# Performance work log

Measured on AMD Instinct MI355X. Metric: run time of the kernel, lower is better.

## Reference

```python
import jax, jax.numpy as jnp
import numpy as np

CH = 64
SCALE = 2
GROUPS = 4
K = 3
GN_GROUPS = min(CH // 8, 8)  # = 8
EPS_GN = 1e-5
EPS_COS = 1e-8


def setup_inputs() -> dict:
    key = jax.random.key(0)
    ks = jax.random.split(key, 4)
    B, H, W = 8, 256, 256
    OC = 2 * GROUPS
    lap = jnp.array([[0., -1., 0.], [-1., 4., -1.], [0., -1., 0.]], dtype=jnp.float32)
    hp_weight = jnp.tile(lap[None, None], (CH, 1, 1, 1))  # depthwise high-pass kernel
    return {
        "x": jax.random.normal(ks[0], (B, CH, H, W), dtype=jnp.float32),
        "gn_gamma": jnp.ones((CH,), jnp.float32),
        "gn_beta": jnp.zeros((CH,), jnp.float32),
        "hp_weight": hp_weight,
        "dir_w": jax.random.normal(ks[1], (OC, K * K - 1), jnp.float32) * 0.001,
        "dir_b": jnp.zeros((OC,), jnp.float32),
        "mag_w": jax.random.normal(ks[2], (OC, CH), jnp.float32) * 0.02,
        "mag_b": jnp.zeros((OC,), jnp.float32),
        "hfg_w": jax.random.normal(ks[3], (OC, CH), jnp.float32) * 0.02,
        "hfg_b": jnp.zeros((OC,), jnp.float32),
    }


def group_norm(x, gamma, beta, g, eps=EPS_GN):
    B, C, H, W = x.shape
    xr = x.reshape(B, g, -1)
    mu = xr.mean(-1, keepdims=True)
    var = xr.var(-1, keepdims=True)
    xn = ((xr - mu) * jax.lax.rsqrt(var + eps)).reshape(B, C, H, W)
    return xn * gamma[None, :, None, None] + beta[None, :, None, None]


def dw_conv3(x, w):
    # depthwise 3x3, padding=1, no bias
    return jax.lax.conv_general_dilated(
        x, w, window_strides=(1, 1), padding=((1, 1), (1, 1)),
        dimension_numbers=("NCHW", "OIHW", "NCHW"), feature_group_count=x.shape[1])


def avg_pool(x, s):
    B, C, H, W = x.shape
    return x.reshape(B, C, H // s, s, W // s, s).mean(axis=(3, 5))


def direction_feat(x, k=K):
    # cosine similarity (over channels) of center pixel vs each of k*k neighbors, center dropped
    B, C, H, W = x.shape
    p = k // 2
    xp = jnp.pad(x, ((0, 0), (0, 0), (p, p), (p, p)))
    patches = jnp.stack([xp[:, :, i:i + H, j:j + W]
                         for i in range(k) for j in range(k)], axis=2)  # [B,C,k2,H,W]
    center = patches[:, :, k * k // 2:k * k // 2 + 1]  # [B,C,1,H,W]
    dot = (center * patches).sum(axis=1)               # [B,k2,H,W]
    n1 = jnp.sqrt((center * center).sum(axis=1))       # [B,1,H,W]
    n2 = jnp.sqrt((patches * patches).sum(axis=1))     # [B,k2,H,W]
    sim = dot / (jnp.maximum(n1, EPS_COS) * jnp.maximum(n2, EPS_COS))
    c = k * k // 2
    return jnp.concatenate([sim[:, :c], sim[:, c + 1:]], axis=1)  # [B,k2-1,H,W]


def conv1x1(w, b, x):
    return jnp.einsum("oc,bchw->bohw", w, x) + b[None, :, None, None]


def grid_sample_border(x, grid):
    # x: [N,C,H,W]; grid: [N,Hg,Wg,2] in [-1,1]; bilinear, align_corners=False, padding_mode='border'
    N, C, H, W = x.shape
    gx, gy = grid[..., 0], grid[..., 1]
    ix = jnp.clip(((gx + 1.0) * W - 1.0) * 0.5, 0.0, W - 1.0)
    iy = jnp.clip(((gy + 1.0) * H - 1.0) * 0.5, 0.0, H - 1.0)
    x0 = jnp.floor(ix); y0 = jnp.floor(iy)
    wx = (ix - x0)[..., None]; wy = (iy - y0)[..., None]
    x0i = jnp.clip(x0.astype(jnp.int32), 0, W - 1)
    y0i = jnp.clip(y0.astype(jnp.int32), 0, H - 1)
    x1i = jnp.clip(x0i + 1, 0, W - 1)
    y1i = jnp.clip(y0i + 1, 0, H - 1)
    img = x.transpose(0, 2, 3, 1)  # [N,H,W,C]
    b = jnp.arange(N)[:, None, None]
    v00 = img[b, y0i, x0i]; v01 = img[b, y0i, x1i]
    v10 = img[b, y1i, x0i]; v11 = img[b, y1i, x1i]
    out = (v00 * (1 - wx) * (1 - wy) + v01 * wx * (1 - wy)
           + v10 * (1 - wx) * wy + v11 * wx * wy)
    return out.transpose(0, 3, 1, 2)  # [N,C,Hg,Wg]


def reference(x, gn_gamma, gn_beta, hp_weight, dir_w, dir_b, mag_w, mag_b, hfg_w, hfg_b):
    B, C, H, W = x.shape
    xn = group_norm(x, gn_gamma, gn_beta, GN_GROUPS)
    hf = dw_conv3(xn, hp_weight)
    xl = avg_pool(xn, SCALE)
    hfl = avg_pool(hf, SCALE)
    df = direction_feat(xl)
    gate = jax.nn.sigmoid(conv1x1(mag_w, mag_b, xl) + conv1x1(hfg_w, hfg_b, hfl))
    offset = conv1x1(dir_w, dir_b, df) * gate  # [B, 2*GROUPS, Hl, Wl]
    Hl, Wl = H // SCALE, W // SCALE
    off = offset.reshape(B, 2, GROUPS, Hl, Wl)
    cy = jnp.arange(Hl, dtype=x.dtype) * SCALE + SCALE / 2.0  # high-res pixel centers
    cx = jnp.arange(Wl, dtype=x.dtype) * SCALE + SCALE / 2.0
    gx = (cx[None, None, None, :] + off[:, 0]) * (2.0 / W) - 1.0  # [B,G,Hl,Wl]
    gy = (cy[None, None, :, None] + off[:, 1]) * (2.0 / H) - 1.0
    grid = jnp.stack([gx, gy], axis=-1).reshape(B * GROUPS, Hl, Wl, 2)
    xg = x.reshape(B * GROUPS, C // GROUPS, H, W)
    out = grid_sample_border(xg, grid)
    return out.reshape(B, C, Hl, Wl)
```

## Files before the change

kernel.cpp:

```cpp
#include <hip/hip_runtime.h>
#include <hip/hip_bf16.h>
#include <math.h>

#define B_ 8
#define C_ 64
#define H_ 256
#define W_ 256
#define HL_ 128
#define WL_ 128
#define GN_G 8
#define CPG 8
#define GRP 4
#define OC_ 8
#define GROUP_ELEMS (CPG * H_ * W_)

#define TILE_H 16
#define XROWS 34
#define LDSW 264

__global__ __launch_bounds__(256) void k2_fused(const float* __restrict__ x,
                                                const float* __restrict__ hpw,
                                                float* __restrict__ px,
                                                float* __restrict__ pL,
                                                float* __restrict__ partials) {
  __shared__ float tile[XROWS * LDSW];
  __shared__ float rs[4], rs2[4];
  const int t = threadIdx.x;
  const int blk = blockIdx.x;
  const int tileIdx = blk & 7;
  const int bc = blk >> 3;
  const int c = bc & 63;
  const int hl0 = tileIdx * TILE_H;
  const float* plane = x + (size_t)bc * (H_ * W_);
  const int y0 = 2 * hl0 - 1;

  if (t < XROWS * 2) {
    const int r = t >> 1;
    tile[r * LDSW + ((t & 1) ? 260 : 3)] = 0.f;
  }

  float s = 0.f, s2 = 0.f;
  for (int i = 0; i < 9; ++i) {
    const int q = t + i * 256;
    if (q >= XROWS * 64) break;
    const int r = q >> 6;
    const int c4 = (q & 63) << 2;
    const int y = y0 + r;
    float4 v = make_float4(0.f, 0.f, 0.f, 0.f);
    if ((unsigned)y < (unsigned)H_)
      v = *reinterpret_cast<const float4*>(plane + y * W_ + c4);
    *reinterpret_cast<float4*>(&tile[r * LDSW + 4 + c4]) = v;
    if (r >= 1 && r <= 32) {
      s  += v.x + v.y + v.z + v.w;
      s2 += v.x * v.x + v.y * v.y + v.z * v.z + v.w * v.w;
    }
  }
#pragma unroll
  for (int off = 32; off > 0; off >>= 1) {
    s  += __shfl_down(s, off, 64);
    s2 += __shfl_down(s2, off, 64);
  }
  if ((t & 63) == 0) { rs[t >> 6] = s; rs2[t >> 6] = s2; }
  __syncthreads();
  if (t == 0) {
    partials[blk * 2 + 0] = rs[0] + rs[1] + rs[2] + rs[3];
    partials[blk * 2 + 1] = rs2[0] + rs2[1] + rs2[2] + rs2[3];
  }

  float w[9];
#pragma unroll
  for (int i = 0; i < 9; ++i) w[i] = hpw[c * 9 + i];

  const int wl = t & 127;
  const int hs = (t >> 7) * 8;
  const int colb = 3 + 2 * wl;
  const int rbase = 2 * hs;
  float win[4][4];
#pragma unroll
  for (int j = 0; j < 4; ++j)
#pragma unroll
    for (int d = 0; d < 4; ++d)
      win[j][d] = tile[(rbase + j) * LDSW + colb + d];

  int outIdx = (bc * HL_ + (hl0 + hs)) * WL_ + wl;
#pragma unroll
  for (int i = 0; i < 8; ++i) {
    float pr[4][3];
#pragma unroll
    for (int j = 0; j < 4; ++j)
#pragma unroll
      for (int d = 0; d < 3; ++d) pr[j][d] = win[j][d] + win[j][d + 1];
    float hfsum = 0.f;
    float q11 = 0.f;
#pragma unroll
    for (int j = 0; j < 3; ++j)
#pragma unroll
      for (int d = 0; d < 3; ++d) {
        const float qq = pr[j][d] + pr[j + 1][d];
        hfsum = fmaf(w[j * 3 + d], qq, hfsum);
        if (j == 1 && d == 1) q11 = qq;
      }
    px[outIdx] = 0.25f * q11;
    pL[outIdx] = 0.25f * hfsum;
    outIdx += WL_;
    if (i < 7) {
      const int rn = rbase + 2 * i + 4;
#pragma unroll
      for (int d = 0; d < 4; ++d) {
        win[0][d] = win[2][d];
        win[1][d] = win[3][d];
        win[2][d] = tile[rn * LDSW + colb + d];
        win[3][d] = tile[(rn + 1) * LDSW + colb + d];
      }
    }
  }
}

__global__ __launch_bounds__(512) void k1_finish(const float* __restrict__ partials,
                                                 const float* __restrict__ gamma,
                                                 const float* __restrict__ beta,
                                                 float* __restrict__ ab) {
  const int t = threadIdx.x;
  const int b = t >> 6, c = t & 63, g = c >> 3;
  float S = 0.f, S2 = 0.f;
  for (int c2 = g * CPG; c2 < g * CPG + CPG; ++c2)
#pragma unroll
    for (int p = 0; p < 8; ++p) {
      const int blk = (b * 64 + c2) * 8 + p;
      S  += partials[blk * 2 + 0];
      S2 += partials[blk * 2 + 1];
    }
  const float N = (float)GROUP_ELEMS;
  const float mean = S / N;
  const float var = fmaxf(S2 / N - mean * mean, 0.f);
  const float a = rsqrtf(var + 1e-5f) * gamma[c];
  ab[t * 2 + 0] = a;
  ab[t * 2 + 1] = beta[c] - mean * a;
}

#define TS 16
__global__ __launch_bounds__(256) void k3_offset(const float* __restrict__ px,
                                                 const float* __restrict__ pL,
                                                 const float* __restrict__ ab,
                                                 const float* __restrict__ dir_w,
                                                 const float* __restrict__ dir_b,
                                                 const float* __restrict__ mag_w,
                                                 const float* __restrict__ mag_b,
                                                 const float* __restrict__ hfg_w,
                                                 const float* __restrict__ hfg_b,
                                                 float2* __restrict__ grid) {
  __shared__ float s_v[2][16][18][24];
  __shared__ float s_mw[C_][OC_];
  __shared__ float s_hw[C_][OC_];
  __shared__ float s_dir[OC_][8];
  __shared__ float s_ab2[C_][2];
  __shared__ float s_bias[2][OC_];

  const int tid = threadIdx.x;
  const int bx = blockIdx.x;
  const int tx = bx & 7, ty = (bx >> 3) & 7, b = bx >> 6;
  const int hl0 = ty * TS, wl0 = tx * TS;
  const size_t planeSz = (size_t)HL_ * WL_;

  for (int i = tid; i < OC_ * C_; i += 256) {
    const int o = i >> 6, c = i & 63;
    s_mw[c][o] = mag_w[i];
    s_hw[c][o] = hfg_w[i];
  }
  if (tid < 64) s_dir[tid >> 3][tid & 7] = dir_w[tid];
  if (tid < 128) s_ab2[tid >> 1][tid & 1] = ab[b * 128 + tid];
  if (tid < OC_) { s_bias[0][tid] = mag_b[tid] + hfg_b[tid]; s_bias[1][tid] = dir_b[tid]; }
  __syncthreads();

  auto stage = [&](int cc, int sel) {
    for (int q = tid; q < 16 * 18 * 6; q += 256) {
      const int c = q / 108, rem = q % 108, r = rem / 6, f4 = rem % 6;
      const int cg = cc * 16 + c;
      const int gy = hl0 - 1 + r;
      const int gx0 = wl0 - 4 + f4 * 4;
      const float a = s_ab2[cg][0], bb = s_ab2[cg][1];
      const float* pp = px + (size_t)(b * C_ + cg) * planeSz + gy * WL_ + gx0;
      float4 v = make_float4(0.f, 0.f, 0.f, 0.f);
      if ((unsigned)gy < (unsigned)HL_) {
        if (gx0 >= 0 && gx0 + 3 < WL_) {
          v = *reinterpret_cast<const float4*>(pp);
          v.x = fmaf(a, v.x, bb); v.y = fmaf(a, v.y, bb);
          v.z = fmaf(a, v.z, bb); v.w = fmaf(a, v.w, bb);
        } else {
          if ((unsigned)(gx0 + 0) < (unsigned)WL_) v.x = fmaf(a, pp[0], bb);
          if ((unsigned)(gx0 + 1) < (unsigned)WL_) v.y = fmaf(a, pp[1], bb);
          if ((unsigned)(gx0 + 2) < (unsigned)WL_) v.z = fmaf(a, pp[2], bb);
          if ((unsigned)(gx0 + 3) < (unsigned)WL_) v.w = fmaf(a, pp[3], bb);
        }
      }
      *reinterpret_cast<float4*>(&s_v[sel][c][r][f4 * 4]) = v;
    }
  };

  const int pxi = tid & 15, pyi = tid >> 4;
  const int hl = hl0 + pyi, wl = wl0 + pxi;
  const float mterm = 0.5f * ((hl == 0) + (hl == HL_ - 1) + (wl == 0) + (wl == WL_ - 1));

  float dot[8], n2[8], z[8], n1 = 0.f;
#pragma unroll
  for (int k = 0; k < 8; ++k) { dot[k] = 0.f; n2[k] = 0.f; z[k] = 0.f; }

  stage(0, 0);
  __syncthreads();

  for (int cc = 0; cc < 4; ++cc) {
    if (cc < 3) stage(cc + 1, (cc + 1) & 1);
    const int sel = cc & 1;
    float lh[16];
    const size_t pbase = (size_t)(b * C_ + cc * 16) * planeSz + hl * WL_ + wl;
#pragma unroll
    for (int c = 0; c < 16; ++c) lh[c] = pL[pbase + c * planeSz];
#pragma unroll
    for (int c = 0; c < 16; ++c) {
      const int cg = cc * 16 + c;
      const float a = s_ab2[cg][0], bb = s_ab2[cg][1];
      const float vc = s_v[sel][c][pyi + 1][pxi + 4];
      const float vh = fmaf(a, lh[c], bb * mterm);
      n1 = fmaf(vc, vc, n1);
      const float u0 = s_v[sel][c][pyi][pxi + 3];
      const float u1 = s_v[sel][c][pyi][pxi + 4];
      const float u2 = s_v[sel][c][pyi][pxi + 5];
      const float u3 = s_v[sel][c][pyi + 1][pxi + 3];
      const float u4 = s_v[sel][c][pyi + 1][pxi + 5];
      const float u5 = s_v[sel][c][pyi + 2][pxi + 3];
      const float u6 = s_v[sel][c][pyi + 2][pxi + 4];
      const float u7 = s_v[sel][c][pyi + 2][pxi + 5];
      dot[0] = fmaf(vc, u0, dot[0]); n2[0] = fmaf(u0, u0, n2[0]);
      dot[1] = fmaf(vc, u1, dot[1]); n2[1] = fmaf(u1, u1, n2[1]);
      dot[2] = fmaf(vc, u2, dot[2]); n2[2] = fmaf(u2, u2, n2[2]);
      dot[3] = fmaf(vc, u3, dot[3]); n2[3] = fmaf(u3, u3, n2[3]);
      dot[4] = fmaf(vc, u4, dot[4]); n2[4] = fmaf(u4, u4, n2[4]);
      dot[5] = fmaf(vc, u5, dot[5]); n2[5] = fmaf(u5, u5, n2[5]);
      dot[6] = fmaf(vc, u6, dot[6]); n2[6] = fmaf(u6, u6, n2[6]);
      dot[7] = fmaf(vc, u7, dot[7]); n2[7] = fmaf(u7, u7, n2[7]);
      const float4 mw0 = *reinterpret_cast<const float4*>(&s_mw[cg][0]);
      const float4 mw1 = *reinterpret_cast<const float4*>(&s_mw[cg][4]);
      const float4 hw0 = *reinterpret_cast<const float4*>(&s_hw[cg][0]);
      const float4 hw1 = *reinterpret_cast<const float4*>(&s_hw[cg][4]);
      z[0] = fmaf(mw0.x, vc, fmaf(hw0.x, vh, z[0]));
      z[1] = fmaf(mw0.y, vc, fmaf(hw0.y, vh, z[1]));
      z[2] = fmaf(mw0.z, vc, fmaf(hw0.z, vh, z[2]));
      z[3] = fmaf(mw0.w, vc, fmaf(hw0.w, vh, z[3]));
      z[4] = fmaf(mw1.x, vc, fmaf(hw1.x, vh, z[4]));
      z[5] = fmaf(mw1.y, vc, fmaf(hw1.y, vh, z[5]));
      z[6] = fmaf(mw1.z, vc, fmaf(hw1.z, vh, z[6]));
      z[7] = fmaf(mw1.w, vc, fmaf(hw1.w, vh, z[7]));
    }
    __syncthreads();
  }

  const float n1c = fmaxf(sqrtf(n1), 1e-8f);
  float df[8];
#pragma unroll
  for (int k = 0; k < 8; ++k)
    df[k] = dot[k] / (n1c * fmaxf(sqrtf(n2[k]), 1e-8f));

  float off[8];
#pragma unroll
  for (int o = 0; o < 8; ++o) {
    float t1 = s_bias[1][o];
#pragma unroll
    for (int j = 0; j < 8; ++j) t1 = fmaf(s_dir[o][j], df[j], t1);
    const float zz = z[o] + s_bias[0][o];
    off[o] = t1 / (1.f + expf(-zz));
  }

#pragma unroll
  for (int g = 0; g < GRP; ++g) {
    const float ix = fminf(fmaxf(2.f * wl + 0.5f + off[g], 0.f), (float)(W_ - 1));
    const float iy = fminf(fmaxf(2.f * hl + 0.5f + off[GRP + g], 0.f), (float)(H_ - 1));
    grid[(b * GRP + g) * (HL_ * WL_) + hl * WL_ + wl] = make_float2(ix, iy);
  }
}

__global__ __launch_bounds__(256) void k4_sample(const float* __restrict__ x,
                                                 const float2* __restrict__ grid,
                                                 float* __restrict__ out) {
  const int idx = blockIdx.x * 256 + threadIdx.x;
  const int wl = idx & (WL_ - 1);
  const int hl = (idx >> 7) & (HL_ - 1);
  const int qc = (idx >> 14) & 3;
  const int g = (idx >> 16) & 3;
  const int b = idx >> 18;
  const float2 G = grid[(b * GRP + g) * (HL_ * WL_) + hl * WL_ + wl];
  const float ix = G.x, iy = G.y;
  const float x0f = floorf(ix), y0f = floorf(iy);
  const float wx = ix - x0f, wy = iy - y0f;
  const int x0 = (int)x0f, y0 = (int)y0f;
  const int x1 = min(x0 + 1, W_ - 1), y1 = min(y0 + 1, H_ - 1);
  const float w00 = (1.f - wx) * (1.f - wy), w01 = wx * (1.f - wy);
  const float w10 = (1.f - wx) * wy,        w11 = wx * wy;
  const int c0 = g * 16 + qc * 4;
  const float* plane = x + (size_t)(b * C_ + c0) * (H_ * W_);
  float* po = out + (size_t)(b * C_ + c0) * (HL_ * WL_) + hl * WL_ + wl;
#pragma unroll
  for (int j = 0; j < 4; ++j) {
    const float v00 = plane[y0 * W_ + x0];
    const float v01 = plane[y0 * W_ + x1];
    const float v10 = plane[y1 * W_ + x0];
    const float v11 = plane[y1 * W_ + x1];
    *po = fmaf(v00, w00, fmaf(v01, w01, fmaf(v10, w10, v11 * w11)));
    plane += H_ * W_;
    po += HL_ * WL_;
  }
}

extern "C" void kernel_launch(void* const* d_in, const int* in_sizes, int n_in,
                              void* d_out, int out_size, void* d_ws, size_t ws_size,
                              hipStream_t stream) {
  const float* x = (const float*)d_in[0];
  const float* gn_gamma = (const float*)d_in[1];
  const float* gn_beta = (const float*)d_in[2];
  const float* hp_weight = (const float*)d_in[3];
  const float* dir_w = (const float*)d_in[4];
  const float* dir_b = (const float*)d_in[5];
  const float* mag_w = (const float*)d_in[6];
  const float* mag_b = (const float*)d_in[7];
  const float* hfg_w = (const float*)d_in[8];
  const float* hfg_b = (const float*)d_in[9];
  float* out = (float*)d_out;

  float* ws = (float*)d_ws;
  float* partials = ws;
  float* ab = ws + 8192;
  float* px = ws + 16384;
  float* pL = px + (size_t)B_ * C_ * HL_ * WL_;
  float2* grid = (float2*)(pL + (size_t)B_ * C_ * HL_ * WL_);

  k2_fused<<<B_ * C_ * 8, 256, 0, stream>>>(x, hp_weight, px, pL, partials);
  k1_finish<<<1, 512, 0, stream>>>(partials, gn_gamma, gn_beta, ab);
  k3_offset<<<B_ * (HL_ / TS) * (WL_ / TS), 256, 0, stream>>>(px, pL, ab, dir_w, dir_b,
                                                              mag_w, mag_b, hfg_w, hfg_b, grid);
  k4_sample<<<(B_ * GRP * 4 * HL_ * WL_) / 256, 256, 0, stream>>>(x, grid, out);
}
```

Baseline: 104.5 us.

## Split k3 channels across thread pairs, register-staged prefetch, vectorized bilinear taps

k3_offset now launches 512 threads per tile, with each output pixel handled by two threads that split the channels and then combine their partial sums with a shuffle. The next channel chunk is loaded into registers before compute and written to LDS after it, so global latency can overlap with the math. k4_sample gets a fast path that reads each pair of horizontal taps as one float2 when the base coordinates are even, falling back to scalar loads otherwise. The cost is more register pressure from the staging buffers and a divergent branch in the sampler.

```diff
diff --git a/kernel.cpp b/kernel.cpp
--- a/kernel.cpp
+++ b/kernel.cpp
@@ -139,16 +139,17 @@
 }
 
 #define TS 16
-__global__ __launch_bounds__(256) void k3_offset(const float* __restrict__ px,
-                                                 const float* __restrict__ pL,
-                                                 const float* __restrict__ ab,
-                                                 const float* __restrict__ dir_w,
-                                                 const float* __restrict__ dir_b,
-                                                 const float* __restrict__ mag_w,
-                                                 const float* __restrict__ mag_b,
-                                                 const float* __restrict__ hfg_w,
-                                                 const float* __restrict__ hfg_b,
-                                                 float2* __restrict__ grid) {
+#define NSTG 4
+__global__ __launch_bounds__(512, 4) void k3_offset(const float* __restrict__ px,
+                                                    const float* __restrict__ pL,
+                                                    const float* __restrict__ ab,
+                                                    const float* __restrict__ dir_w,
+                                                    const float* __restrict__ dir_b,
+                                                    const float* __restrict__ mag_w,
+                                                    const float* __restrict__ mag_b,
+                                                    const float* __restrict__ hfg_w,
+                                                    const float* __restrict__ hfg_b,
+                                                    float2* __restrict__ grid) {
   __shared__ float s_v[2][16][18][24];
   __shared__ float s_mw[C_][OC_];
   __shared__ float s_hw[C_][OC_];
@@ -162,42 +163,61 @@
   const int hl0 = ty * TS, wl0 = tx * TS;
   const size_t planeSz = (size_t)HL_ * WL_;
 
-  for (int i = tid; i < OC_ * C_; i += 256) {
-    const int o = i >> 6, c = i & 63;
-    s_mw[c][o] = mag_w[i];
-    s_hw[c][o] = hfg_w[i];
+  {
+    const int i = tid;
+    s_mw[i & 63][i >> 6] = mag_w[i];
+    s_hw[i & 63][i >> 6] = hfg_w[i];
   }
   if (tid < 64) s_dir[tid >> 3][tid & 7] = dir_w[tid];
   if (tid < 128) s_ab2[tid >> 1][tid & 1] = ab[b * 128 + tid];
   if (tid < OC_) { s_bias[0][tid] = mag_b[tid] + hfg_b[tid]; s_bias[1][tid] = dir_b[tid]; }
-  __syncthreads();
-
-  auto stage = [&](int cc, int sel) {
-    for (int q = tid; q < 16 * 18 * 6; q += 256) {
+
+  auto issue = [&](int cc, float4 (&reg)[NSTG]) {
+#pragma unroll
+    for (int i = 0; i < NSTG; ++i) {
+      const int q = tid + i * 512;
+      if (q >= 16 * 18 * 6) continue;
+      const int c = q / 108, rem = q % 108, r = rem / 6, f4 = rem % 6;
+      const int cg = cc * 16 + c;
+      const int gy = hl0 - 1 + r;
+      const int gx0 = wl0 - 4 + f4 * 4;
+      float4 v = make_float4(0.f, 0.f, 0.f, 0.f);
+      if ((unsigned)gy < (unsigned)HL_) {
+        const float* pp = px + (size_t)(b * C_ + cg) * planeSz + gy * WL_ + gx0;
+        if (gx0 >= 0 && gx0 + 3 < WL_) {
+          v = *reinterpret_cast<const float4*>(pp);
+        } else {
+          if ((unsigned)(gx0 + 0) < (unsigned)WL_) v.x = pp[0];
+          if ((unsigned)(gx0 + 1) < (unsigned)WL_) v.y = pp[1];
+          if ((unsigned)(gx0 + 2) < (unsigned)WL_) v.z = pp[2];
+          if ((unsigned)(gx0 + 3) < (unsigned)WL_) v.w = pp[3];
+        }
+      }
+      reg[i] = v;
+    }
+  };
+  auto commit = [&](int cc, int sel, float4 (&reg)[NSTG]) {
+#pragma unroll
+    for (int i = 0; i < NSTG; ++i) {
+      const int q = tid + i * 512;
+      if (q >= 16 * 18 * 6) continue;
       const int c = q / 108, rem = q % 108, r = rem / 6, f4 = rem % 6;
       const int cg = cc * 16 + c;
       const int gy = hl0 - 1 + r;
       const int gx0 = wl0 - 4 + f4 * 4;
       const float a = s_ab2[cg][0], bb = s_ab2[cg][1];
-      const float* pp = px + (size_t)(b * C_ + cg) * planeSz + gy * WL_ + gx0;
-      float4 v = make_float4(0.f, 0.f, 0.f, 0.f);
-      if ((unsigned)gy < (unsigned)HL_) {
-        if (gx0 >= 0 && gx0 + 3 < WL_) {
-          v = *reinterpret_cast<const float4*>(pp);
-          v.x = fmaf(a, v.x, bb); v.y = fmaf(a, v.y, bb);
-          v.z = fmaf(a, v.z, bb); v.w = fmaf(a, v.w, bb);
-        } else {
-          if ((unsigned)(gx0 + 0) < (unsigned)WL_) v.x = fmaf(a, pp[0], bb);
-          if ((unsigned)(gx0 + 1) < (unsigned)WL_) v.y = fmaf(a, pp[1], bb);
-          if ((unsigned)(gx0 + 2) < (unsigned)WL_) v.z = fmaf(a, pp[2], bb);
-          if ((unsigned)(gx0 + 3) < (unsigned)WL_) v.w = fmaf(a, pp[3], bb);
-        }
-      }
+      const bool rok = (unsigned)gy < (unsigned)HL_;
+      float4 v = reg[i];
+      v.x = (rok && (unsigned)(gx0 + 0) < (unsigned)WL_) ? fmaf(a, v.x, bb) : 0.f;
+      v.y = (rok && (unsigned)(gx0 + 1) < (unsigned)WL_) ? fmaf(a, v.y, bb) : 0.f;
+      v.z = (rok && (unsigned)(gx0 + 2) < (unsigned)WL_) ? fmaf(a, v.z, bb) : 0.f;
+      v.w = (rok && (unsigned)(gx0 + 3) < (unsigned)WL_) ? fmaf(a, v.w, bb) : 0.f;
       *reinterpret_cast<float4*>(&s_v[sel][c][r][f4 * 4]) = v;
     }
   };
 
-  const int pxi = tid & 15, pyi = tid >> 4;
+  const int p = tid >> 1, cg = tid & 1;
+  const int pxi = p & 15, pyi = p >> 4;
   const int hl = hl0 + pyi, wl = wl0 + pxi;
   const float mterm = 0.5f * ((hl == 0) + (hl == HL_ - 1) + (wl == 0) + (wl == WL_ - 1));
 
@@ -205,31 +225,36 @@
 #pragma unroll
   for (int k = 0; k < 8; ++k) { dot[k] = 0.f; n2[k] = 0.f; z[k] = 0.f; }
 
-  stage(0, 0);
+  float4 sreg[NSTG];
+  issue(0, sreg);
   __syncthreads();
+  commit(0, 0, sreg);
+  __syncthreads();
 
   for (int cc = 0; cc < 4; ++cc) {
-    if (cc < 3) stage(cc + 1, (cc + 1) & 1);
     const int sel = cc & 1;
-    float lh[16];
-    const size_t pbase = (size_t)(b * C_ + cc * 16) * planeSz + hl * WL_ + wl;
-#pragma unroll
-    for (int c = 0; c < 16; ++c) lh[c] = pL[pbase + c * planeSz];
-#pragma unroll
-    for (int c = 0; c < 16; ++c) {
-      const int cg = cc * 16 + c;
-      const float a = s_ab2[cg][0], bb = s_ab2[cg][1];
-      const float vc = s_v[sel][c][pyi + 1][pxi + 4];
-      const float vh = fmaf(a, lh[c], bb * mterm);
+    float lh[8];
+    const size_t lbase = (size_t)(b * C_ + cc * 16 + cg) * planeSz + hl * WL_ + wl;
+#pragma unroll
+    for (int jj = 0; jj < 8; ++jj) lh[jj] = pL[lbase + 2 * jj * planeSz];
+    if (cc < 3) issue(cc + 1, sreg);
+
+#pragma unroll
+    for (int jj = 0; jj < 8; ++jj) {
+      const int cl = 2 * jj + cg;
+      const int cgc = cc * 16 + cl;
+      const float a = s_ab2[cgc][0], bb = s_ab2[cgc][1];
+      const float vc = s_v[sel][cl][pyi + 1][pxi + 4];
+      const float vh = fmaf(a, lh[jj], bb * mterm);
       n1 = fmaf(vc, vc, n1);
-      const float u0 = s_v[sel][c][pyi][pxi + 3];
-      const float u1 = s_v[sel][c][pyi][pxi + 4];
-      const float u2 = s_v[sel][c][pyi][pxi + 5];
-      const float u3 = s_v[sel][c][pyi + 1][pxi + 3];
-      const float u4 = s_v[sel][c][pyi + 1][pxi + 5];
-      const float u5 = s_v[sel][c][pyi + 2][pxi + 3];
-      const float u6 = s_v[sel][c][pyi + 2][pxi + 4];
-      const float u7 = s_v[sel][c][pyi + 2][pxi + 5];
+      const float u0 = s_v[sel][cl][pyi][pxi + 3];
+      const float u1 = s_v[sel][cl][pyi][pxi + 4];
+      const float u2 = s_v[sel][cl][pyi][pxi + 5];
+      const float u3 = s_v[sel][cl][pyi + 1][pxi + 3];
+      const float u4 = s_v[sel][cl][pyi + 1][pxi + 5];
+      const float u5 = s_v[sel][cl][pyi + 2][pxi + 3];
+      const float u6 = s_v[sel][cl][pyi + 2][pxi + 4];
+      const float u7 = s_v[sel][cl][pyi + 2][pxi + 5];
       dot[0] = fmaf(vc, u0, dot[0]); n2[0] = fmaf(u0, u0, n2[0]);
       dot[1] = fmaf(vc, u1, dot[1]); n2[1] = fmaf(u1, u1, n2[1]);
       dot[2] = fmaf(vc, u2, dot[2]); n2[2] = fmaf(u2, u2, n2[2]);
@@ -238,10 +263,10 @@
       dot[5] = fmaf(vc, u5, dot[5]); n2[5] = fmaf(u5, u5, n2[5]);
       dot[6] = fmaf(vc, u6, dot[6]); n2[6] = fmaf(u6, u6, n2[6]);
       dot[7] = fmaf(vc, u7, dot[7]); n2[7] = fmaf(u7, u7, n2[7]);
-      const float4 mw0 = *reinterpret_cast<const float4*>(&s_mw[cg][0]);
-      const float4 mw1 = *reinterpret_cast<const float4*>(&s_mw[cg][4]);
-      const float4 hw0 = *reinterpret_cast<const float4*>(&s_hw[cg][0]);
-      const float4 hw1 = *reinterpret_cast<const float4*>(&s_hw[cg][4]);
+      const float4 mw0 = *reinterpret_cast<const float4*>(&s_mw[cgc][0]);
+      const float4 mw1 = *reinterpret_cast<const float4*>(&s_mw[cgc][4]);
+      const float4 hw0 = *reinterpret_cast<const float4*>(&s_hw[cgc][0]);
+      const float4 hw1 = *reinterpret_cast<const float4*>(&s_hw[cgc][4]);
       z[0] = fmaf(mw0.x, vc, fmaf(hw0.x, vh, z[0]));
       z[1] = fmaf(mw0.y, vc, fmaf(hw0.y, vh, z[1]));
       z[2] = fmaf(mw0.z, vc, fmaf(hw0.z, vh, z[2]));
@@ -251,8 +276,19 @@
       z[6] = fmaf(mw1.z, vc, fmaf(hw1.z, vh, z[6]));
       z[7] = fmaf(mw1.w, vc, fmaf(hw1.w, vh, z[7]));
     }
-    __syncthreads();
-  }
+    if (cc < 3) {
+      commit(cc + 1, sel ^ 1, sreg);
+      __syncthreads();
+    }
+  }
+
+#pragma unroll
+  for (int k = 0; k < 8; ++k) {
+    dot[k] += __shfl_xor(dot[k], 1);
+    n2[k]  += __shfl_xor(n2[k], 1);
+    z[k]   += __shfl_xor(z[k], 1);
+  }
+  n1 += __shfl_xor(n1, 1);
 
   const float n1c = fmaxf(sqrtf(n1), 1e-8f);
   float df[8];
@@ -260,21 +296,20 @@
   for (int k = 0; k < 8; ++k)
     df[k] = dot[k] / (n1c * fmaxf(sqrtf(n2[k]), 1e-8f));
 
-  float off[8];
-#pragma unroll
-  for (int o = 0; o < 8; ++o) {
-    float t1 = s_bias[1][o];
-#pragma unroll
-    for (int j = 0; j < 8; ++j) t1 = fmaf(s_dir[o][j], df[j], t1);
-    const float zz = z[o] + s_bias[0][o];
-    off[o] = t1 / (1.f + expf(-zz));
-  }
-
-#pragma unroll
-  for (int g = 0; g < GRP; ++g) {
-    const float ix = fminf(fmaxf(2.f * wl + 0.5f + off[g], 0.f), (float)(W_ - 1));
-    const float iy = fminf(fmaxf(2.f * hl + 0.5f + off[GRP + g], 0.f), (float)(H_ - 1));
-    grid[(b * GRP + g) * (HL_ * WL_) + hl * WL_ + wl] = make_float2(ix, iy);
+#pragma unroll
+  for (int gg = 0; gg < 2; ++gg) {
+    const int o = cg * 2 + gg;
+    float offx = s_bias[1][o], offy = s_bias[1][o + 4];
+#pragma unroll
+    for (int j = 0; j < 8; ++j) {
+      offx = fmaf(s_dir[o][j], df[j], offx);
+      offy = fmaf(s_dir[o + 4][j], df[j], offy);
+    }
+    offx *= 1.f / (1.f + expf(-(z[o] + s_bias[0][o])));
+    offy *= 1.f / (1.f + expf(-(z[o + 4] + s_bias[0][o + 4])));
+    const float ix = fminf(fmaxf(2.f * wl + 0.5f + offx, 0.f), (float)(W_ - 1));
+    const float iy = fminf(fmaxf(2.f * hl + 0.5f + offy, 0.f), (float)(H_ - 1));
+    grid[(b * GRP + o) * (HL_ * WL_) + hl * WL_ + wl] = make_float2(ix, iy);
   }
 }
 
@@ -288,25 +323,36 @@
   const int g = (idx >> 16) & 3;
   const int b = idx >> 18;
   const float2 G = grid[(b * GRP + g) * (HL_ * WL_) + hl * WL_ + wl];
-  const float ix = G.x, iy = G.y;
-  const float x0f = floorf(ix), y0f = floorf(iy);
-  const float wx = ix - x0f, wy = iy - y0f;
+  const float x0f = floorf(G.x), y0f = floorf(G.y);
+  const float wx = G.x - x0f, wy = G.y - y0f;
   const int x0 = (int)x0f, y0 = (int)y0f;
-  const int x1 = min(x0 + 1, W_ - 1), y1 = min(y0 + 1, H_ - 1);
   const float w00 = (1.f - wx) * (1.f - wy), w01 = wx * (1.f - wy);
   const float w10 = (1.f - wx) * wy,        w11 = wx * wy;
   const int c0 = g * 16 + qc * 4;
   const float* plane = x + (size_t)(b * C_ + c0) * (H_ * W_);
   float* po = out + (size_t)(b * C_ + c0) * (HL_ * WL_) + hl * WL_ + wl;
-#pragma unroll
-  for (int j = 0; j < 4; ++j) {
-    const float v00 = plane[y0 * W_ + x0];
-    const float v01 = plane[y0 * W_ + x1];
-    const float v10 = plane[y1 * W_ + x0];
-    const float v11 = plane[y1 * W_ + x1];
-    *po = fmaf(v00, w00, fmaf(v01, w01, fmaf(v10, w10, v11 * w11)));
-    plane += H_ * W_;
-    po += HL_ * WL_;
+
+  if (__builtin_expect(((x0 | y0) & 1) == 0, 1)) {
+#pragma unroll
+    for (int j = 0; j < 4; ++j) {
+      const float2 r0 = *reinterpret_cast<const float2*>(plane + y0 * W_ + x0);
+      const float2 r1 = *reinterpret_cast<const float2*>(plane + (y0 + 1) * W_ + x0);
+      *po = fmaf(r0.x, w00, fmaf(r0.y, w01, fmaf(r1.x, w10, r1.y * w11)));
+      plane += H_ * W_;
+      po += HL_ * WL_;
+    }
+  } else {
+    const int x1 = min(x0 + 1, W_ - 1), y1 = min(y0 + 1, H_ - 1);
+#pragma unroll
+    for (int j = 0; j < 4; ++j) {
+      const float v00 = plane[y0 * W_ + x0];
+      const float v01 = plane[y0 * W_ + x1];
+      const float v10 = plane[y1 * W_ + x0];
+      const float v11 = plane[y1 * W_ + x1];
+      *po = fmaf(v00, w00, fmaf(v01, w01, fmaf(v10, w10, v11 * w11)));
+      plane += H_ * W_;
+      po += HL_ * WL_;
+    }
   }
 }
 
@@ -334,7 +380,7 @@
 
   k2_fused<<<B_ * C_ * 8, 256, 0, stream>>>(x, hp_weight, px, pL, partials);
   k1_finish<<<1, 512, 0, stream>>>(partials, gn_gamma, gn_beta, ab);
-  k3_offset<<<B_ * (HL_ / TS) * (WL_ / TS), 256, 0, stream>>>(px, pL, ab, dir_w, dir_b,
+  k3_offset<<<B_ * (HL_ / TS) * (WL_ / TS), 512, 0, stream>>>(px, pL, ab, dir_w, dir_b,
                                                               mag_w, mag_b, hfg_w, hfg_b, grid);
   k4_sample<<<(B_ * GRP * 4 * HL_ * WL_) / 256, 256, 0, stream>>>(x, grid, out);
 }
```

After: 405.0 us. 288% more time.

## Split offset kernel channels across 4 lanes with 8x8 tiles; vectorize sampling loads

Applied to the files above, without the earlier changes.

The offset kernel now uses 8x8 pixel tiles with four threads per pixel, each handling a quarter of the channels, and combines partial sums with wave shuffles. Each thread then writes one group's grid entry, and the 4x larger launch grid gives more blocks for occupancy. The double-buffered LDS staging is replaced by single-buffer staging with two barriers per chunk, which gives up load/compute overlap and re-reads more halo data. The sample kernel adds a fast path that uses float2 loads when the sample corner is even-aligned, falling back to scalar loads otherwise.

```diff
diff --git a/kernel.cpp b/kernel.cpp
--- a/kernel.cpp
+++ b/kernel.cpp
@@ -138,7 +138,6 @@
   ab[t * 2 + 1] = beta[c] - mean * a;
 }
 
-#define TS 16
 __global__ __launch_bounds__(256) void k3_offset(const float* __restrict__ px,
                                                  const float* __restrict__ pL,
                                                  const float* __restrict__ ab,
@@ -149,7 +148,7 @@
                                                  const float* __restrict__ hfg_w,
                                                  const float* __restrict__ hfg_b,
                                                  float2* __restrict__ grid) {
-  __shared__ float s_v[2][16][18][24];
+  __shared__ float s_v[16][10][20];
   __shared__ float s_mw[C_][OC_];
   __shared__ float s_hw[C_][OC_];
   __shared__ float s_dir[OC_][8];
@@ -158,46 +157,20 @@
 
   const int tid = threadIdx.x;
   const int bx = blockIdx.x;
-  const int tx = bx & 7, ty = (bx >> 3) & 7, b = bx >> 6;
-  const int hl0 = ty * TS, wl0 = tx * TS;
+  const int wt = bx & 15, ht = (bx >> 4) & 15, b = bx >> 8;
+  const int hl0 = ht * 8, wl0 = wt * 8;
   const size_t planeSz = (size_t)HL_ * WL_;
 
   for (int i = tid; i < OC_ * C_; i += 256) {
-    const int o = i >> 6, c = i & 63;
-    s_mw[c][o] = mag_w[i];
-    s_hw[c][o] = hfg_w[i];
+    s_mw[i & 63][i >> 6] = mag_w[i];
+    s_hw[i & 63][i >> 6] = hfg_w[i];
   }
   if (tid < 64) s_dir[tid >> 3][tid & 7] = dir_w[tid];
   if (tid < 128) s_ab2[tid >> 1][tid & 1] = ab[b * 128 + tid];
   if (tid < OC_) { s_bias[0][tid] = mag_b[tid] + hfg_b[tid]; s_bias[1][tid] = dir_b[tid]; }
-  __syncthreads();
-
-  auto stage = [&](int cc, int sel) {
-    for (int q = tid; q < 16 * 18 * 6; q += 256) {
-      const int c = q / 108, rem = q % 108, r = rem / 6, f4 = rem % 6;
-      const int cg = cc * 16 + c;
-      const int gy = hl0 - 1 + r;
-      const int gx0 = wl0 - 4 + f4 * 4;
-      const float a = s_ab2[cg][0], bb = s_ab2[cg][1];
-      const float* pp = px + (size_t)(b * C_ + cg) * planeSz + gy * WL_ + gx0;
-      float4 v = make_float4(0.f, 0.f, 0.f, 0.f);
-      if ((unsigned)gy < (unsigned)HL_) {
-        if (gx0 >= 0 && gx0 + 3 < WL_) {
-          v = *reinterpret_cast<const float4*>(pp);
-          v.x = fmaf(a, v.x, bb); v.y = fmaf(a, v.y, bb);
-          v.z = fmaf(a, v.z, bb); v.w = fmaf(a, v.w, bb);
-        } else {
-          if ((unsigned)(gx0 + 0) < (unsigned)WL_) v.x = fmaf(a, pp[0], bb);
-          if ((unsigned)(gx0 + 1) < (unsigned)WL_) v.y = fmaf(a, pp[1], bb);
-          if ((unsigned)(gx0 + 2) < (unsigned)WL_) v.z = fmaf(a, pp[2], bb);
-          if ((unsigned)(gx0 + 3) < (unsigned)WL_) v.w = fmaf(a, pp[3], bb);
-        }
-      }
-      *reinterpret_cast<float4*>(&s_v[sel][c][r][f4 * 4]) = v;
-    }
-  };
-
-  const int pxi = tid & 15, pyi = tid >> 4;
+
+  const int cg = tid & 3, p = tid >> 2;
+  const int pxi = p & 7, pyi = p >> 3;
   const int hl = hl0 + pyi, wl = wl0 + pxi;
   const float mterm = 0.5f * ((hl == 0) + (hl == HL_ - 1) + (wl == 0) + (wl == WL_ - 1));
 
@@ -205,31 +178,60 @@
 #pragma unroll
   for (int k = 0; k < 8; ++k) { dot[k] = 0.f; n2[k] = 0.f; z[k] = 0.f; }
 
-  stage(0, 0);
-  __syncthreads();
-
   for (int cc = 0; cc < 4; ++cc) {
-    if (cc < 3) stage(cc + 1, (cc + 1) & 1);
-    const int sel = cc & 1;
-    float lh[16];
-    const size_t pbase = (size_t)(b * C_ + cc * 16) * planeSz + hl * WL_ + wl;
-#pragma unroll
-    for (int c = 0; c < 16; ++c) lh[c] = pL[pbase + c * planeSz];
-#pragma unroll
-    for (int c = 0; c < 16; ++c) {
-      const int cg = cc * 16 + c;
-      const float a = s_ab2[cg][0], bb = s_ab2[cg][1];
-      const float vc = s_v[sel][c][pyi + 1][pxi + 4];
-      const float vh = fmaf(a, lh[c], bb * mterm);
+    float lh[4];
+#pragma unroll
+    for (int j = 0; j < 4; ++j)
+      lh[j] = pL[(size_t)(b * C_ + cc * 16 + 4 * j + cg) * planeSz + hl * WL_ + wl];
+
+    __syncthreads();
+
+#pragma unroll
+    for (int i = 0; i < 3; ++i) {
+      const int q = tid + i * 256;
+      if (q < 640) {
+        const int c = q / 40;
+        const int rem = q - c * 40;
+        const int r = rem >> 2;
+        const int f4 = rem & 3;
+        const int cgl = cc * 16 + c;
+        const int gy = hl0 - 1 + r;
+        const int gx0 = wl0 - 4 + f4 * 4;
+        const float a = s_ab2[cgl][0], bb = s_ab2[cgl][1];
+        float4 v = make_float4(0.f, 0.f, 0.f, 0.f);
+        if ((unsigned)gy < (unsigned)HL_) {
+          const float* pp = px + (size_t)(b * C_ + cgl) * planeSz + gy * WL_ + gx0;
+          if (gx0 >= 0 && gx0 + 3 < WL_) {
+            const float4 rv = *reinterpret_cast<const float4*>(pp);
+            v.x = fmaf(a, rv.x, bb); v.y = fmaf(a, rv.y, bb);
+            v.z = fmaf(a, rv.z, bb); v.w = fmaf(a, rv.w, bb);
+          } else {
+            if ((unsigned)(gx0 + 0) < (unsigned)WL_) v.x = fmaf(a, pp[0], bb);
+            if ((unsigned)(gx0 + 1) < (unsigned)WL_) v.y = fmaf(a, pp[1], bb);
+            if ((unsigned)(gx0 + 2) < (unsigned)WL_) v.z = fmaf(a, pp[2], bb);
+            if ((unsigned)(gx0 + 3) < (unsigned)WL_) v.w = fmaf(a, pp[3], bb);
+          }
+        }
+        *reinterpret_cast<float4*>(&s_v[c][r][f4 * 4]) = v;
+      }
+    }
+    __syncthreads();
+
+#pragma unroll
+    for (int j = 0; j < 4; ++j) {
+      const int cl = 4 * j + cg;
+      const int cgl = cc * 16 + cl;
+      const float vh = fmaf(s_ab2[cgl][0], lh[j], s_ab2[cgl][1] * mterm);
+      const float vc = s_v[cl][pyi + 1][pxi + 4];
       n1 = fmaf(vc, vc, n1);
-      const float u0 = s_v[sel][c][pyi][pxi + 3];
-      const float u1 = s_v[sel][c][pyi][pxi + 4];
-      const float u2 = s_v[sel][c][pyi][pxi + 5];
-      const float u3 = s_v[sel][c][pyi + 1][pxi + 3];
-      const float u4 = s_v[sel][c][pyi + 1][pxi + 5];
-      const float u5 = s_v[sel][c][pyi + 2][pxi + 3];
-      const float u6 = s_v[sel][c][pyi + 2][pxi + 4];
-      const float u7 = s_v[sel][c][pyi + 2][pxi + 5];
+      const float u0 = s_v[cl][pyi][pxi + 3];
+      const float u1 = s_v[cl][pyi][pxi + 4];
+      const float u2 = s_v[cl][pyi][pxi + 5];
+      const float u3 = s_v[cl][pyi + 1][pxi + 3];
+      const float u4 = s_v[cl][pyi + 1][pxi + 5];
+      const float u5 = s_v[cl][pyi + 2][pxi + 3];
+      const float u6 = s_v[cl][pyi + 2][pxi + 4];
+      const float u7 = s_v[cl][pyi + 2][pxi + 5];
       dot[0] = fmaf(vc, u0, dot[0]); n2[0] = fmaf(u0, u0, n2[0]);
       dot[1] = fmaf(vc, u1, dot[1]); n2[1] = fmaf(u1, u1, n2[1]);
       dot[2] = fmaf(vc, u2, dot[2]); n2[2] = fmaf(u2, u2, n2[2]);
@@ -238,10 +240,10 @@
       dot[5] = fmaf(vc, u5, dot[5]); n2[5] = fmaf(u5, u5, n2[5]);
       dot[6] = fmaf(vc, u6, dot[6]); n2[6] = fmaf(u6, u6, n2[6]);
       dot[7] = fmaf(vc, u7, dot[7]); n2[7] = fmaf(u7, u7, n2[7]);
-      const float4 mw0 = *reinterpret_cast<const float4*>(&s_mw[cg][0]);
-      const float4 mw1 = *reinterpret_cast<const float4*>(&s_mw[cg][4]);
-      const float4 hw0 = *reinterpret_cast<const float4*>(&s_hw[cg][0]);
-      const float4 hw1 = *reinterpret_cast<const float4*>(&s_hw[cg][4]);
+      const float4 mw0 = *reinterpret_cast<const float4*>(&s_mw[cgl][0]);
+      const float4 mw1 = *reinterpret_cast<const float4*>(&s_mw[cgl][4]);
+      const float4 hw0 = *reinterpret_cast<const float4*>(&s_hw[cgl][0]);
+      const float4 hw1 = *reinterpret_cast<const float4*>(&s_hw[cgl][4]);
       z[0] = fmaf(mw0.x, vc, fmaf(hw0.x, vh, z[0]));
       z[1] = fmaf(mw0.y, vc, fmaf(hw0.y, vh, z[1]));
       z[2] = fmaf(mw0.z, vc, fmaf(hw0.z, vh, z[2]));
@@ -251,8 +253,15 @@
       z[6] = fmaf(mw1.z, vc, fmaf(hw1.z, vh, z[6]));
       z[7] = fmaf(mw1.w, vc, fmaf(hw1.w, vh, z[7]));
     }
-    __syncthreads();
-  }
+  }
+
+#pragma unroll
+  for (int k = 0; k < 8; ++k) {
+    dot[k] += __shfl_xor(dot[k], 1); dot[k] += __shfl_xor(dot[k], 2);
+    n2[k]  += __shfl_xor(n2[k], 1);  n2[k]  += __shfl_xor(n2[k], 2);
+    z[k]   += __shfl_xor(z[k], 1);   z[k]   += __shfl_xor(z[k], 2);
+  }
+  n1 += __shfl_xor(n1, 1); n1 += __shfl_xor(n1, 2);
 
   const float n1c = fmaxf(sqrtf(n1), 1e-8f);
   float df[8];
@@ -260,22 +269,20 @@
   for (int k = 0; k < 8; ++k)
     df[k] = dot[k] / (n1c * fmaxf(sqrtf(n2[k]), 1e-8f));
 
-  float off[8];
-#pragma unroll
-  for (int o = 0; o < 8; ++o) {
-    float t1 = s_bias[1][o];
-#pragma unroll
-    for (int j = 0; j < 8; ++j) t1 = fmaf(s_dir[o][j], df[j], t1);
-    const float zz = z[o] + s_bias[0][o];
-    off[o] = t1 / (1.f + expf(-zz));
-  }
-
-#pragma unroll
-  for (int g = 0; g < GRP; ++g) {
-    const float ix = fminf(fmaxf(2.f * wl + 0.5f + off[g], 0.f), (float)(W_ - 1));
-    const float iy = fminf(fmaxf(2.f * hl + 0.5f + off[GRP + g], 0.f), (float)(H_ - 1));
-    grid[(b * GRP + g) * (HL_ * WL_) + hl * WL_ + wl] = make_float2(ix, iy);
-  }
+  float offx = s_bias[1][cg], offy = s_bias[1][cg + 4];
+#pragma unroll
+  for (int jj = 0; jj < 8; ++jj) {
+    offx = fmaf(s_dir[cg][jj], df[jj], offx);
+    offy = fmaf(s_dir[cg + 4][jj], df[jj], offy);
+  }
+  const float zx = ((cg == 0) ? z[0] : (cg == 1) ? z[1] : (cg == 2) ? z[2] : z[3]) + s_bias[0][cg];
+  const float zy = ((cg == 0) ? z[4] : (cg == 1) ? z[5] : (cg == 2) ? z[6] : z[7]) + s_bias[0][cg + 4];
+  offx *= 1.f / (1.f + expf(-zx));
+  offy *= 1.f / (1.f + expf(-zy));
+
+  const float ix = fminf(fmaxf(2.f * wl + 0.5f + offx, 0.f), (float)(W_ - 1));
+  const float iy = fminf(fmaxf(2.f * hl + 0.5f + offy, 0.f), (float)(H_ - 1));
+  grid[(b * GRP + cg) * (HL_ * WL_) + hl * WL_ + wl] = make_float2(ix, iy);
 }
 
 __global__ __launch_bounds__(256) void k4_sample(const float* __restrict__ x,
@@ -288,25 +295,36 @@
   const int g = (idx >> 16) & 3;
   const int b = idx >> 18;
   const float2 G = grid[(b * GRP + g) * (HL_ * WL_) + hl * WL_ + wl];
-  const float ix = G.x, iy = G.y;
-  const float x0f = floorf(ix), y0f = floorf(iy);
-  const float wx = ix - x0f, wy = iy - y0f;
+  const float x0f = floorf(G.x), y0f = floorf(G.y);
+  const float wx = G.x - x0f, wy = G.y - y0f;
   const int x0 = (int)x0f, y0 = (int)y0f;
-  const int x1 = min(x0 + 1, W_ - 1), y1 = min(y0 + 1, H_ - 1);
   const float w00 = (1.f - wx) * (1.f - wy), w01 = wx * (1.f - wy);
   const float w10 = (1.f - wx) * wy,        w11 = wx * wy;
   const int c0 = g * 16 + qc * 4;
   const float* plane = x + (size_t)(b * C_ + c0) * (H_ * W_);
   float* po = out + (size_t)(b * C_ + c0) * (HL_ * WL_) + hl * WL_ + wl;
-#pragma unroll
-  for (int j = 0; j < 4; ++j) {
-    const float v00 = plane[y0 * W_ + x0];
-    const float v01 = plane[y0 * W_ + x1];
-    const float v10 = plane[y1 * W_ + x0];
-    const float v11 = plane[y1 * W_ + x1];
-    *po = fmaf(v00, w00, fmaf(v01, w01, fmaf(v10, w10, v11 * w11)));
-    plane += H_ * W_;
-    po += HL_ * WL_;
+
+  if (__builtin_expect(((x0 | y0) & 1) == 0, 1)) {
+#pragma unroll
+    for (int j = 0; j < 4; ++j) {
+      const float2 r0 = *reinterpret_cast<const float2*>(plane + y0 * W_ + x0);
+      const float2 r1 = *reinterpret_cast<const float2*>(plane + (y0 + 1) * W_ + x0);
+      *po = fmaf(r0.x, w00, fmaf(r0.y, w01, fmaf(r1.x, w10, r1.y * w11)));
+      plane += H_ * W_;
+      po += HL_ * WL_;
+    }
+  } else {
+    const int x1 = min(x0 + 1, W_ - 1), y1 = min(y0 + 1, H_ - 1);
+#pragma unroll
+    for (int j = 0; j < 4; ++j) {
+      const float v00 = plane[y0 * W_ + x0];
+      const float v01 = plane[y0 * W_ + x1];
+      const float v10 = plane[y1 * W_ + x0];
+      const float v11 = plane[y1 * W_ + x1];
+      *po = fmaf(v00, w00, fmaf(v01, w01, fmaf(v10, w10, v11 * w11)));
+      plane += H_ * W_;
+      po += HL_ * WL_;
+    }
   }
 }
 
@@ -334,7 +352,7 @@
 
   k2_fused<<<B_ * C_ * 8, 256, 0, stream>>>(x, hp_weight, px, pL, partials);
   k1_finish<<<1, 512, 0, stream>>>(partials, gn_gamma, gn_beta, ab);
-  k3_offset<<<B_ * (HL_ / TS) * (WL_ / TS), 256, 0, stream>>>(px, pL, ab, dir_w, dir_b,
-                                                              mag_w, mag_b, hfg_w, hfg_b, grid);
+  k3_offset<<<B_ * (HL_ / 8) * (WL_ / 8), 256, 0, stream>>>(px, pL, ab, dir_w, dir_b,
+                                                            mag_w, mag_b, hfg_w, hfg_b, grid);
   k4_sample<<<(B_ * GRP * 4 * HL_ * WL_) / 256, 256, 0, stream>>>(x, grid, out);
 }
```

Result: slower. 123.1 us (+17.8%).
